# Kernel optimization log

Measured on AMD Instinct MI355X. Metric: run time of the kernel, lower is better.

The kernel has to match this reference:

```python
import jax, jax.numpy as jnp
import numpy as np

B, S, D_IN, D_OUT = 4, 4096, 2048, 2048
NUM_ADAPTERS, RANK = 8, 16


def setup_inputs() -> dict:
    key = jax.random.key(0)
    ks = jax.random.split(key, 7)
    x = jax.random.normal(ks[0], (B, S, D_IN), dtype=jnp.float32)
    # adapter ids per token in [0, NUM_ADAPTERS]; 0 means 'no adapter'
    lora_mapping = jax.random.randint(ks[1], (B * S,), 0, NUM_ADAPTERS + 1, dtype=jnp.int32)
    weight = jax.random.normal(ks[2], (D_OUT, D_IN), dtype=jnp.float32) * (D_IN ** -0.5)
    bias = jax.random.normal(ks[3], (D_OUT,), dtype=jnp.float32) * 0.01
    # stacked adapters: aid a (1-indexed in mapping) lives at row a-1
    lora_a = jax.random.normal(ks[4], (NUM_ADAPTERS, RANK, D_IN), dtype=jnp.float32) * (D_IN ** -0.5)
    lora_b = jax.random.normal(ks[5], (NUM_ADAPTERS, D_OUT, RANK), dtype=jnp.float32) * (RANK ** -0.5)
    scaling = jnp.full((NUM_ADAPTERS,), 2.0, dtype=jnp.float32)
    return {"x": x, "lora_mapping": lora_mapping, "weight": weight, "bias": bias,
            "lora_a": lora_a, "lora_b": lora_b, "scaling": scaling}


def reference(x, lora_mapping, weight, bias, lora_a, lora_b, scaling):
    # Base dense linear: res = x @ W^T + b
    res = jnp.einsum('bsd,od->bso', x, weight) + bias  # [B,S,D_OUT]
    n_adapters = lora_a.shape[0]
    x2 = x.reshape(-1, x.shape[-1])                    # [N, D_IN]
    # one_hot(aid-1): aid==0 maps to -1 -> all-zero row (adapter skipped),
    # matching the torch loop that ignores aid 0. Fold scaling in here.
    sel = jax.nn.one_hot(lora_mapping - 1, n_adapters, dtype=x.dtype) * scaling  # [N, A]
    # Batched gather-matmul-scatter expressed as dense-over-adapters einsum:
    # u[n,a,r] = x[n] @ la[a]^T ; masked/scaled by sel ; delta[n] = sum_a u[n,a] @ lb[a]^T
    u = jnp.einsum('nd,ard->nar', x2, lora_a) * sel[..., None]  # [N, A, R]
    delta = jnp.einsum('nar,aor->no', u, lora_b)                # [N, D_OUT]
    return res + delta.reshape(res.shape)
```

## Files before the change

### kernel.cpp

```cpp
#include <hip/hip_runtime.h>
#include <hip/hip_bf16.h>


#define D_IN   2048
#define D_OUT  2048
#define NTOK   16384
#define RANK   16
#define NADAPT 8
#define KEXT   2176
#define BM     128
#define BN     128
#define BK     64
#define NROWS  (NTOK + D_OUT)

typedef __attribute__((ext_vector_type(8))) __bf16 bf16x8;
typedef __attribute__((ext_vector_type(8))) unsigned short u16x8;
typedef __attribute__((ext_vector_type(4))) float  f32x4;

__device__ inline unsigned short f2bf(float f) {
    unsigned u = __builtin_bit_cast(unsigned, f);
    u += 0x7fffu + ((u >> 16) & 1u);
    return (unsigned short)(u >> 16);
}

__global__ void conv_la(const float4* __restrict__ la, ushort4* __restrict__ La) {
    int t = blockIdx.x * 256 + threadIdx.x;
    float4 v = la[t];
    ushort4 s;
    s.x = f2bf(v.x); s.y = f2bf(v.y); s.z = f2bf(v.z); s.w = f2bf(v.w);
    La[t] = s;
}

__global__ void conv_all(const float* __restrict__ x, const float* __restrict__ w,
                         unsigned short* __restrict__ XeWe) {
    const size_t TOTAL = (size_t)NROWS * (D_IN / 8);
    size_t stride = (size_t)gridDim.x * blockDim.x;
    for (size_t u = (size_t)blockIdx.x * blockDim.x + threadIdx.x; u < TOTAL; u += stride) {
        int n  = (int)(u >> 8);
        int kc = ((int)u & 255) * 8;
        const float* src = (n < NTOK) ? x + (size_t)n * D_IN + kc
                                      : w + (size_t)(n - NTOK) * D_IN + kc;
        float4 v0 = *(const float4*)(src);
        float4 v1 = *(const float4*)(src + 4);
        u16x8 s;
        s[0] = f2bf(v0.x); s[1] = f2bf(v0.y); s[2] = f2bf(v0.z); s[3] = f2bf(v0.w);
        s[4] = f2bf(v1.x); s[5] = f2bf(v1.y); s[6] = f2bf(v1.z); s[7] = f2bf(v1.w);
        *(u16x8*)(XeWe + (size_t)n * KEXT + kc) = s;
    }
}

__global__ void ext_w(const float* __restrict__ lora_b, unsigned short* __restrict__ We) {
    int t = blockIdx.x * 256 + threadIdx.x;
    int o = t >> 7, c = t & 127;
    int a = c >> 4, r = c & 15;
    We[(size_t)o * KEXT + D_IN + c] = f2bf(lora_b[((size_t)a * D_OUT + o) * RANK + r]);
}

__global__ void ext_mfma(unsigned short* Xe, const int* __restrict__ map,
                         const unsigned short* __restrict__ La,
                         const float* __restrict__ scaling) {
    int t = threadIdx.x, lane = t & 63, wave = t >> 6;
    int n0 = blockIdx.x * 32;
    int arow = lane & 15;
    int kq   = lane >> 4;

    f32x4 acc[2] = {};

    const unsigned short* xr0 = Xe + (size_t)(n0 + arow) * KEXT + kq * 8;
    const unsigned short* xr1 = xr0 + (size_t)16 * KEXT;
    const unsigned short* lb  = La + (size_t)(wave * 16 + arow) * D_IN + kq * 8;

#pragma unroll 4
    for (int k0 = 0; k0 < D_IN; k0 += 32) {
        bf16x8 a0 = *(const bf16x8*)(xr0 + k0);
        bf16x8 a1 = *(const bf16x8*)(xr1 + k0);
        bf16x8 b  = *(const bf16x8*)(lb + k0);
        acc[0] = __builtin_amdgcn_mfma_f32_16x16x32_bf16(a0, b, acc[0], 0, 0, 0);
        acc[1] = __builtin_amdgcn_mfma_f32_16x16x32_bf16(a1, b, acc[1], 0, 0, 0);
    }

    int colq = lane & 15, rq = lane >> 4;
    int c = wave * 16 + colq;
    float sc = scaling[wave];
#pragma unroll
    for (int i = 0; i < 2; ++i) {
#pragma unroll
        for (int r = 0; r < 4; ++r) {
            int token = n0 + i * 16 + rq * 4 + r;
            unsigned short v = 0;
            if (map[token] == wave + 1) v = f2bf(acc[i][r] * sc);
            Xe[(size_t)token * KEXT + D_IN + c] = v;
        }
    }
}

__global__ void gemm_fused(const unsigned short* __restrict__ Xe,
                           const unsigned short* __restrict__ We,
                           const float* __restrict__ bias,
                           float* __restrict__ out) {
    __shared__ unsigned short As[BM * BK];
    __shared__ unsigned short Bs[BN * BK];

    int t = threadIdx.x;
    int lane = t & 63, wave = t >> 6;
    int g = blockIdx.x;
    int group = g >> 7, within = g & 127;
    int bm = group * 8 + (within & 7);
    int bn = within >> 3;

    int wm = wave >> 1, wn = wave & 1;
    f32x4 acc[4][4] = {};

    for (int k0 = 0; k0 < KEXT; k0 += BK) {
        __syncthreads();
#pragma unroll
        for (int c = 0; c < 4; ++c) {
            int linear = (wave * 4 + c) * 64 + lane;
            int row = linear >> 3;
            int kc  = linear & 7;
            int gc  = kc ^ (row & 7);
            const unsigned short* ga = Xe + (size_t)(bm * BM + row) * KEXT + k0 + gc * 8;
            __builtin_amdgcn_global_load_lds(
                (const __attribute__((address_space(1))) unsigned int*)ga,
                (__attribute__((address_space(3))) unsigned int*)(As + (wave * 4 + c) * 512),
                16, 0, 0);
            const unsigned short* gb = We + (size_t)(bn * BN + row) * KEXT + k0 + gc * 8;
            __builtin_amdgcn_global_load_lds(
                (const __attribute__((address_space(1))) unsigned int*)gb,
                (__attribute__((address_space(3))) unsigned int*)(Bs + (wave * 4 + c) * 512),
                16, 0, 0);
        }
        __syncthreads();
#pragma unroll
        for (int ks = 0; ks < 2; ++ks) {
            bf16x8 af[4], bfr[4];
            int gchunk = ks * 4 + (lane >> 4);
            int sw = gchunk ^ (lane & 7);
#pragma unroll
            for (int i = 0; i < 4; ++i) {
                int rowA = wm * 64 + i * 16 + (lane & 15);
                af[i]  = *(const bf16x8*)(As + rowA * BK + sw * 8);
                int rowB = wn * 64 + i * 16 + (lane & 15);
                bfr[i] = *(const bf16x8*)(Bs + rowB * BK + sw * 8);
            }
#pragma unroll
            for (int i = 0; i < 4; ++i)
#pragma unroll
                for (int j = 0; j < 4; ++j)
                    acc[i][j] = __builtin_amdgcn_mfma_f32_16x16x32_bf16(af[i], bfr[j], acc[i][j], 0, 0, 0);
        }
    }

    int colq = lane & 15, rq = lane >> 4;
#pragma unroll
    for (int j = 0; j < 4; ++j) {
        int col = bn * BN + wn * 64 + j * 16 + colq;
        float bv = bias[col];
#pragma unroll
        for (int i = 0; i < 4; ++i) {
            int row0 = bm * BM + wm * 64 + i * 16 + rq * 4;
#pragma unroll
            for (int r = 0; r < 4; ++r)
                out[(size_t)(row0 + r) * D_OUT + col] = acc[i][j][r] + bv;
        }
    }
}

extern "C" void kernel_launch(void* const* d_in, const int* in_sizes, int n_in,
                              void* d_out, int out_size, void* d_ws, size_t ws_size,
                              hipStream_t stream) {
    (void)in_sizes; (void)n_in; (void)out_size; (void)ws_size;
    const float* x       = (const float*)d_in[0];
    const int*   map     = (const int*)d_in[1];
    const float* weight  = (const float*)d_in[2];
    const float* bias    = (const float*)d_in[3];
    const float* lora_a  = (const float*)d_in[4];
    const float* lora_b  = (const float*)d_in[5];
    const float* scaling = (const float*)d_in[6];
    float* out = (float*)d_out;

    unsigned short* Xe = (unsigned short*)d_ws;
    unsigned short* We = Xe + (size_t)NTOK * KEXT;
    unsigned short* La = We + (size_t)D_OUT * KEXT;

    conv_la<<<256, 256, 0, stream>>>((const float4*)lora_a, (ushort4*)La);
    conv_all<<<2304, 256, 0, stream>>>(x, weight, Xe);
    ext_w<<<1024, 256, 0, stream>>>(lora_b, We);
    ext_mfma<<<NTOK / 32, 512, 0, stream>>>(Xe, map, La, scaling);
    gemm_fused<<<(NTOK / BM) * (D_OUT / BN), 256, 0, stream>>>(Xe, We, bias, out);
}
```

Before: 463.8 us.

## Merge conversion kernels into one prep launch and stage LoRA-A GEMM through LDS

Result: faster. 400.1 us (-13.7%).

```diff
diff --git a/kernel.cpp b/kernel.cpp
--- a/kernel.cpp
+++ b/kernel.cpp
@@ -11,7 +11,7 @@
 #define BM     128
 #define BN     128
 #define BK     64
-#define NROWS  (NTOK + D_OUT)
+#define EBM    32
 
 typedef __attribute__((ext_vector_type(8))) __bf16 bf16x8;
 typedef __attribute__((ext_vector_type(8))) unsigned short u16x8;
@@ -23,73 +23,114 @@
     return (unsigned short)(u >> 16);
 }
 
-__global__ void conv_la(const float4* __restrict__ la, ushort4* __restrict__ La) {
-    int t = blockIdx.x * 256 + threadIdx.x;
-    float4 v = la[t];
-    ushort4 s;
-    s.x = f2bf(v.x); s.y = f2bf(v.y); s.z = f2bf(v.z); s.w = f2bf(v.w);
-    La[t] = s;
-}
-
-__global__ void conv_all(const float* __restrict__ x, const float* __restrict__ w,
-                         unsigned short* __restrict__ XeWe) {
-    const size_t TOTAL = (size_t)NROWS * (D_IN / 8);
-    size_t stride = (size_t)gridDim.x * blockDim.x;
-    for (size_t u = (size_t)blockIdx.x * blockDim.x + threadIdx.x; u < TOTAL; u += stride) {
-        int n  = (int)(u >> 8);
-        int kc = ((int)u & 255) * 8;
-        const float* src = (n < NTOK) ? x + (size_t)n * D_IN + kc
-                                      : w + (size_t)(n - NTOK) * D_IN + kc;
+#define SEG0 ((size_t)NTOK * 256)
+#define SEG1 (SEG0 + (size_t)D_OUT * 256)
+#define SEG2 (SEG1 + 32768)
+#define TOTU (SEG2 + 32768)
+
+__global__ void conv_prep(const float* __restrict__ x, const float* __restrict__ w,
+                          const float* __restrict__ la, const float* __restrict__ lb,
+                          unsigned short* __restrict__ Xe, unsigned short* __restrict__ We,
+                          unsigned short* __restrict__ La) {
+    size_t stride = (size_t)gridDim.x * 256;
+    for (size_t u = (size_t)blockIdx.x * 256 + threadIdx.x; u < TOTU; u += stride) {
+        const float* src;
+        unsigned short* dst;
+        if (u < SEG0) {
+            int n = (int)(u >> 8), kc = ((int)u & 255) * 8;
+            src = x + (size_t)n * D_IN + kc;
+            dst = Xe + (size_t)n * KEXT + kc;
+        } else if (u < SEG1) {
+            size_t v = u - SEG0;
+            int o = (int)(v >> 8), kc = ((int)v & 255) * 8;
+            src = w + (size_t)o * D_IN + kc;
+            dst = We + (size_t)o * KEXT + kc;
+        } else if (u < SEG2) {
+            size_t v = u - SEG1;
+            src = la + v * 8;
+            dst = La + v * 8;
+        } else {
+            size_t v = u - SEG2;
+            int o = (int)(v >> 4), m = (int)v & 15;
+            int a = m >> 1, r = (m & 1) * 8;
+            src = lb + ((size_t)a * D_OUT + o) * RANK + r;
+            dst = We + (size_t)o * KEXT + D_IN + m * 8;
+        }
         float4 v0 = *(const float4*)(src);
         float4 v1 = *(const float4*)(src + 4);
         u16x8 s;
         s[0] = f2bf(v0.x); s[1] = f2bf(v0.y); s[2] = f2bf(v0.z); s[3] = f2bf(v0.w);
         s[4] = f2bf(v1.x); s[5] = f2bf(v1.y); s[6] = f2bf(v1.z); s[7] = f2bf(v1.w);
-        *(u16x8*)(XeWe + (size_t)n * KEXT + kc) = s;
-    }
-}
-
-__global__ void ext_w(const float* __restrict__ lora_b, unsigned short* __restrict__ We) {
-    int t = blockIdx.x * 256 + threadIdx.x;
-    int o = t >> 7, c = t & 127;
-    int a = c >> 4, r = c & 15;
-    We[(size_t)o * KEXT + D_IN + c] = f2bf(lora_b[((size_t)a * D_OUT + o) * RANK + r]);
-}
-
-__global__ void ext_mfma(unsigned short* Xe, const int* __restrict__ map,
+        *(u16x8*)dst = s;
+    }
+}
+
+__global__ void ext_gemm(unsigned short* Xe, const int* __restrict__ map,
                          const unsigned short* __restrict__ La,
                          const float* __restrict__ scaling) {
+    __shared__ unsigned short As[EBM * BK];
+    __shared__ unsigned short Bs[128 * BK];
+
     int t = threadIdx.x, lane = t & 63, wave = t >> 6;
-    int n0 = blockIdx.x * 32;
-    int arow = lane & 15;
-    int kq   = lane >> 4;
-
-    f32x4 acc[2] = {};
-
-    const unsigned short* xr0 = Xe + (size_t)(n0 + arow) * KEXT + kq * 8;
-    const unsigned short* xr1 = xr0 + (size_t)16 * KEXT;
-    const unsigned short* lb  = La + (size_t)(wave * 16 + arow) * D_IN + kq * 8;
-
-#pragma unroll 4
-    for (int k0 = 0; k0 < D_IN; k0 += 32) {
-        bf16x8 a0 = *(const bf16x8*)(xr0 + k0);
-        bf16x8 a1 = *(const bf16x8*)(xr1 + k0);
-        bf16x8 b  = *(const bf16x8*)(lb + k0);
-        acc[0] = __builtin_amdgcn_mfma_f32_16x16x32_bf16(a0, b, acc[0], 0, 0, 0);
-        acc[1] = __builtin_amdgcn_mfma_f32_16x16x32_bf16(a1, b, acc[1], 0, 0, 0);
+    int n0 = blockIdx.x * EBM;
+
+    f32x4 acc[2][2] = {};
+
+    for (int k0 = 0; k0 < D_IN; k0 += BK) {
+        __syncthreads();
+        {
+            int row = t >> 3, kc = t & 7, gc = kc ^ (row & 7);
+            const unsigned short* ga = Xe + (size_t)(n0 + row) * KEXT + k0 + gc * 8;
+            __builtin_amdgcn_global_load_lds(
+                (const __attribute__((address_space(1))) unsigned int*)ga,
+                (__attribute__((address_space(3))) unsigned int*)(As + wave * 512),
+                16, 0, 0);
+        }
+#pragma unroll
+        for (int c = 0; c < 4; ++c) {
+            int linear = (wave * 4 + c) * 64 + lane;
+            int row = linear >> 3, kc = linear & 7, gc = kc ^ (row & 7);
+            const unsigned short* gb = La + (size_t)row * D_IN + k0 + gc * 8;
+            __builtin_amdgcn_global_load_lds(
+                (const __attribute__((address_space(1))) unsigned int*)gb,
+                (__attribute__((address_space(3))) unsigned int*)(Bs + (wave * 4 + c) * 512),
+                16, 0, 0);
+        }
+        __syncthreads();
+#pragma unroll
+        for (int ks = 0; ks < 2; ++ks) {
+            int gchunk = ks * 4 + (lane >> 4);
+            int sw = gchunk ^ (lane & 7);
+            bf16x8 af[2], bfr[2];
+#pragma unroll
+            for (int i = 0; i < 2; ++i)
+                af[i] = *(const bf16x8*)(As + (i * 16 + (lane & 15)) * BK + sw * 8);
+#pragma unroll
+            for (int j = 0; j < 2; ++j)
+                bfr[j] = *(const bf16x8*)(Bs + (wave * 32 + j * 16 + (lane & 15)) * BK + sw * 8);
+#pragma unroll
+            for (int i = 0; i < 2; ++i)
+#pragma unroll
+                for (int j = 0; j < 2; ++j)
+                    acc[i][j] = __builtin_amdgcn_mfma_f32_16x16x32_bf16(af[i], bfr[j], acc[i][j], 0, 0, 0);
+        }
     }
 
     int colq = lane & 15, rq = lane >> 4;
-    int c = wave * 16 + colq;
-    float sc = scaling[wave];
-#pragma unroll
-    for (int i = 0; i < 2; ++i) {
-#pragma unroll
-        for (int r = 0; r < 4; ++r) {
-            int token = n0 + i * 16 + rq * 4 + r;
-            unsigned short v = 0;
-            if (map[token] == wave + 1) v = f2bf(acc[i][r] * sc);
-            Xe[(size_t)token * KEXT + D_IN + c] = v;
+#pragma unroll
+    for (int j = 0; j < 2; ++j) {
+        int c = wave * 32 + j * 16 + colq;
+        int aid = wave * 2 + j + 1;
+        float sc = scaling[wave * 2 + j];
+#pragma unroll
+        for (int i = 0; i < 2; ++i) {
+#pragma unroll
+            for (int r = 0; r < 4; ++r) {
+                int token = n0 + i * 16 + rq * 4 + r;
+                unsigned short v = 0;
+                if (map[token] == aid) v = f2bf(acc[i][j][r] * sc);
+                Xe[(size_t)token * KEXT + D_IN + c] = v;
+            }
         }
     }
 }
@@ -183,9 +224,7 @@
     unsigned short* We = Xe + (size_t)NTOK * KEXT;
     unsigned short* La = We + (size_t)D_OUT * KEXT;
 
-    conv_la<<<256, 256, 0, stream>>>((const float4*)lora_a, (ushort4*)La);
-    conv_all<<<2304, 256, 0, stream>>>(x, weight, Xe);
-    ext_w<<<1024, 256, 0, stream>>>(lora_b, We);
-    ext_mfma<<<NTOK / 32, 512, 0, stream>>>(Xe, map, La, scaling);
+    conv_prep<<<2048, 256, 0, stream>>>(x, weight, lora_a, lora_b, Xe, We, La);
+    ext_gemm<<<NTOK / EBM, 256, 0, stream>>>(Xe, map, La, scaling);
     gemm_fused<<<(NTOK / BM) * (D_OUT / BN), 256, 0, stream>>>(Xe, We, bias, out);
 }
```
